# Kernel optimization log

Measured on AMD Instinct MI355X. Metric: run time of the kernel, lower is better.

## Reference

```python
import jax, jax.numpy as jnp
import numpy as np

B, S, HID = 2, 1024, 4096
H, KV, D = 32, 8, 128
EPS = 1e-6
ROPE_THETA = 1000000.0


def _make_freqs_cis(seq_len, head_dim, theta):
    inv_freq = 1.0 / (theta ** (jnp.arange(0, head_dim, 2, dtype=jnp.float32) / head_dim))
    ang = jnp.arange(seq_len, dtype=jnp.float32)[:, None] * inv_freq[None, :]  # [S, D/2]
    emb = jnp.concatenate([ang, ang], axis=-1)                                 # [S, D]
    cos, sin = jnp.cos(emb), jnp.sin(emb)
    return jnp.stack([cos, sin, -sin], axis=0)                                 # [3, S, D]


def setup_inputs() -> dict:
    key = jax.random.key(0)
    ks = jax.random.split(key, 8)
    scale = 0.02
    return {
        "hidden_states": jax.random.normal(ks[0], (B, S, HID), dtype=jnp.float32),
        "freqs_cis": _make_freqs_cis(S, D, ROPE_THETA),
        "Wq": jax.random.normal(ks[1], (H * D, HID), dtype=jnp.float32) * scale,
        "Wk": jax.random.normal(ks[2], (KV * D, HID), dtype=jnp.float32) * scale,
        "Wv": jax.random.normal(ks[3], (KV * D, HID), dtype=jnp.float32) * scale,
        "Wo": jax.random.normal(ks[4], (HID, H * D), dtype=jnp.float32) * scale,
        "q_norm_w": jnp.ones((D,), jnp.float32) + jax.random.normal(ks[5], (D,), jnp.float32) * scale,
        "k_norm_w": jnp.ones((D,), jnp.float32) + jax.random.normal(ks[6], (D,), jnp.float32) * scale,
    }


def _rmsnorm(x, w):
    # per-head RMSNorm over last dim (rms_norm_add=False -> plain weight multiply)
    return x * jax.lax.rsqrt(jnp.mean(x * x, axis=-1, keepdims=True) + EPS) * w


def _rope(x, cos, sin, nsin):
    # matches apply_rope: e = x*cos; e[:half] += x[half:]*nsin; e[half:] += x[:half]*sin
    half = x.shape[-1] // 2
    e = x * cos
    lo = e[..., :half] + x[..., half:] * nsin[..., :half]
    hi = e[..., half:] + x[..., :half] * sin[..., half:]
    return jnp.concatenate([lo, hi], axis=-1)


def reference(hidden_states, freqs_cis, Wq, Wk, Wv, Wo, q_norm_w, k_norm_w):
    b, s, _ = hidden_states.shape
    # QKV projections (no bias)
    q = jnp.einsum("bsh,oh->bso", hidden_states, Wq).reshape(b, s, H, D).transpose(0, 2, 1, 3)
    k = jnp.einsum("bsh,oh->bso", hidden_states, Wk).reshape(b, s, KV, D).transpose(0, 2, 1, 3)
    v = jnp.einsum("bsh,oh->bso", hidden_states, Wv).reshape(b, s, KV, D).transpose(0, 2, 1, 3)
    # per-head RMSNorm (Qwen3 'gemma3' q/k norms)
    q = _rmsnorm(q, q_norm_w)
    k = _rmsnorm(k, k_norm_w)
    # RoPE
    cos, sin, nsin = freqs_cis[0], freqs_cis[1], freqs_cis[2]  # [S, D] each, broadcast over (b, heads)
    q = _rope(q, cos, sin, nsin)
    k = _rope(k, cos, sin, nsin)
    # GQA: repeat kv heads to match query heads (repeat_interleave dim=1)
    rep = H // KV
    k = jnp.repeat(k, rep, axis=1)
    v = jnp.repeat(v, rep, axis=1)
    # SDPA (no mask, past_key_value=None path)
    scale = D ** -0.5
    attn = jax.nn.softmax(jnp.einsum("bhqd,bhkd->bhqk", q, k) * scale, axis=-1)
    out = jnp.einsum("bhqk,bhkd->bhqd", attn, v)
    out = out.transpose(0, 2, 1, 3).reshape(b, s, H * D)
    return jnp.einsum("bsi,hi->bsh", out, Wo)
```

## Files before the change

### kernel.cpp

```cpp
#include <hip/hip_runtime.h>


typedef __attribute__((ext_vector_type(8))) short s8v;
typedef __attribute__((ext_vector_type(4))) float f4v;
typedef __attribute__((ext_vector_type(8))) unsigned short u8v;
typedef __attribute__((ext_vector_type(4))) float float4v;
typedef unsigned short us;

#define SB() __builtin_amdgcn_sched_barrier(0)

__device__ __forceinline__ void BARRIER() {
  asm volatile("" ::: "memory");
  __builtin_amdgcn_s_barrier();
  asm volatile("" ::: "memory");
}

__device__ __forceinline__ us f2b(float f) {
  unsigned u = __builtin_bit_cast(unsigned, f);
  u += 0x7fffu + ((u >> 16) & 1u);
  return (us)(u >> 16);
}
__device__ __forceinline__ float b2f(us h) {
  return __builtin_bit_cast(float, (unsigned)h << 16);
}

__device__ __forceinline__ void gload16(const void* g, void* l) {
  __builtin_amdgcn_global_load_lds(
      (const __attribute__((address_space(1))) unsigned int*)g,
      (__attribute__((address_space(3))) unsigned int*)l, 16, 0, 0);
}

__global__ __launch_bounds__(256) void cvt_all_k(const float* __restrict__ h,
                                                 const float* __restrict__ wq,
                                                 const float* __restrict__ wk,
                                                 const float* __restrict__ wv,
                                                 us* __restrict__ dst) {
  long blk = blockIdx.x;
  const float* src;
  long off;
  if (blk < 4096)        { src = h;  off = 0; }
  else if (blk < 12288)  { src = wq; off = 4096; }
  else if (blk < 14336)  { src = wk; off = 12288; }
  else                   { src = wv; off = 14336; }
  long i = (blk - off) * 2048 + (long)threadIdx.x * 8;
  long o = blk * 2048 + (long)threadIdx.x * 8;
  float4v a = *(const float4v*)(src + i);
  float4v b = *(const float4v*)(src + i + 4);
  u8v v;
  v[0] = f2b(a[0]); v[1] = f2b(a[1]); v[2] = f2b(a[2]); v[3] = f2b(a[3]);
  v[4] = f2b(b[0]); v[5] = f2b(b[1]); v[6] = f2b(b[2]); v[7] = f2b(b[3]);
  *(u8v*)(dst + o) = v;
}

__global__ __launch_bounds__(256) void add2_k(const float* __restrict__ p,
                                              float* __restrict__ out, long n) {
  long i = ((long)blockIdx.x * 256 + threadIdx.x) * 8;
  float4v a0 = *(const float4v*)(p + i);
  float4v b0 = *(const float4v*)(p + i + 4);
  float4v a1 = *(const float4v*)(p + n + i);
  float4v b1 = *(const float4v*)(p + n + i + 4);
  float4v ra, rb;
#pragma unroll
  for (int k = 0; k < 4; ++k) { ra[k] = a0[k] + a1[k]; rb[k] = b0[k] + b1[k]; }
  *(float4v*)(out + i) = ra;
  *(float4v*)(out + i + 4) = rb;
}

template <bool F32OUT, bool SPLITK, bool CVTTAIL>
__global__ __launch_bounds__(512, 2) void gemm8p(const us* __restrict__ A,
                                                 const us* __restrict__ W,
                                                 void* __restrict__ Cv,
                                                 int Kfull, int nkt, int ldc,
                                                 int NX, int nGemm,
                                                 const float* __restrict__ csrc,
                                                 us* __restrict__ cdst) {
  if constexpr (CVTTAIL) {
    if ((int)blockIdx.x >= nGemm) {
      long c = (long)((int)blockIdx.x - nGemm) * 512 + threadIdx.x;
      for (; c < 2097152; c += 64 * 512) {
        long i = c * 8;
        float4v x = *(const float4v*)(csrc + i);
        float4v y = *(const float4v*)(csrc + i + 4);
        u8v v;
        v[0] = f2b(x[0]); v[1] = f2b(x[1]); v[2] = f2b(x[2]); v[3] = f2b(x[3]);
        v[4] = f2b(y[0]); v[5] = f2b(y[1]); v[6] = f2b(y[2]); v[7] = f2b(y[3]);
        *(u8v*)(cdst + i) = v;
      }
      return;
    }
  }

  __shared__ __align__(16) us Ah[2][2][128 * 64];
  __shared__ __align__(16) us Bh[2][2][128 * 64];
  const int tid = threadIdx.x, lane = tid & 63, w = tid >> 6;
  const int wr = w >> 2, wc = w & 3;
  const int lr = lane & 15, lg = lane >> 4;

  const int cpx = nGemm >> 3;
  const int swz = ((int)blockIdx.x & 7) * cpx + ((int)blockIdx.x >> 3);
  long m0, n0, koff = 0;
  float* Cks = (float*)Cv;
  if constexpr (SPLITK) {
    const int ks = swz >> 7;
    const int r = swz & 127;
    m0 = (long)(r >> 4) * 256;
    n0 = (long)(r & 15) * 256;
    koff = (long)ks * nkt * 64;
    Cks += (long)ks * 2048 * 4096;
  } else {
    m0 = (long)(swz / NX) * 256;
    n0 = (long)(swz % NX) * 256;
  }

  const int c0 = tid, c1 = 512 + tid;
  const int r0 = c0 >> 3, r1 = c1 >> 3;
  const int s0 = ((c0 & 7) ^ (r0 & 7)) << 3;
  const int s1 = ((c1 & 7) ^ (r1 & 7)) << 3;

#define STG(dst, src)                                                   \
  do {                                                                  \
    const us* _s = (src);                                               \
    us* _d = (dst);                                                     \
    gload16(_s + (long)r0 * Kfull + s0, _d + c0 * 8);                   \
    gload16(_s + (long)r1 * Kfull + s1, _d + c1 * 8);                   \
  } while (0)

  const us* Asrc = A + m0 * Kfull + koff;
  const us* Bsrc = W + n0 * Kfull + koff;
  const long hK = (long)128 * Kfull;

  const int ra = wr * 64 + lr, rb = wc * 32 + lr;
  const int offA0 = ra * 64 + ((lg ^ (ra & 7)) << 3);
  const int offA1 = ra * 64 + (((4 + lg) ^ (ra & 7)) << 3);
  const int offB0 = rb * 64 + ((lg ^ (rb & 7)) << 3);
  const int offB1 = rb * 64 + (((4 + lg) ^ (rb & 7)) << 3);

  f4v acc[8][4];
#pragma unroll
  for (int i = 0; i < 8; ++i)
#pragma unroll
    for (int j = 0; j < 4; ++j) acc[i][j] = (f4v){0.f, 0.f, 0.f, 0.f};

  const int nk = nkt;

  STG(Ah[0][0], Asrc);
  STG(Bh[0][0], Bsrc);
  STG(Bh[0][1], Bsrc + hK);
  STG(Ah[0][1], Asrc + hK);
  STG(Ah[1][0], Asrc + 64);
  STG(Bh[1][1], Bsrc + hK + 64);
  STG(Ah[1][1], Asrc + hK + 64);
  asm volatile("s_waitcnt vmcnt(6)" ::: "memory");
  BARRIER();

  s8v a[4][2], b0[2][2], b1[2][2];

#define RD_A(H)                                                         \
  _Pragma("unroll") for (int f = 0; f < 4; ++f) {                       \
    a[f][0] = *(const s8v*)(&Ah[d][H][offA0 + f * 1024]);               \
    a[f][1] = *(const s8v*)(&Ah[d][H][offA1 + f * 1024]);               \
  }
#define RD_B(BB, H)                                                     \
  _Pragma("unroll") for (int g = 0; g < 2; ++g) {                       \
    BB[g][0] = *(const s8v*)(&Bh[d][H][offB0 + g * 1024]);              \
    BB[g][1] = *(const s8v*)(&Bh[d][H][offB1 + g * 1024]);              \
  }
#define QUAD(QM, QN, BB)                                                \
  __builtin_amdgcn_s_setprio(1);                                        \
  _Pragma("unroll") for (int f = 0; f < 4; ++f)                         \
  _Pragma("unroll") for (int g = 0; g < 2; ++g) {                       \
    f4v t = acc[QM * 4 + f][QN * 2 + g];                                \
    t = __builtin_amdgcn_mfma_f32_16x16x32_bf16(a[f][0], BB[g][0], t, 0, 0, 0); \
    t = __builtin_amdgcn_mfma_f32_16x16x32_bf16(a[f][1], BB[g][1], t, 0, 0, 0); \
    acc[QM * 4 + f][QN * 2 + g] = t;                                    \
  }                                                                     \
  __builtin_amdgcn_s_setprio(0);
#define PREMFMA()                                                       \
  BARRIER();                                                            \
  asm volatile("s_waitcnt lgkmcnt(0)" ::: "memory");                    \
  SB();

  for (int kt = 0; kt < nk; ++kt) {
    const int d = kt & 1;
    const long kb2 = (long)(kt + 2) * 64;
    const bool p1 = (kt + 1 < nk), p2 = (kt + 2 < nk);

    RD_A(0)
    RD_B(b0, 0)
    if (p1) STG(Bh[d ^ 1][0], Bsrc + (long)(kt + 1) * 64);
    PREMFMA()
    QUAD(0, 0, b0)
    SB(); BARRIER();

    RD_B(b1, 1)
    if (p2) STG(Ah[d][0], Asrc + kb2);
    PREMFMA()
    QUAD(0, 1, b1)
    SB(); BARRIER();

    RD_A(1)
    if (p2) STG(Bh[d][1], Bsrc + hK + kb2);
    PREMFMA()
    QUAD(1, 1, b1)
    SB(); BARRIER();

    if (p2) STG(Ah[d][1], Asrc + hK + kb2);
    PREMFMA()
    QUAD(1, 0, b0)
    SB();
    if (p2) asm volatile("s_waitcnt vmcnt(6)" ::: "memory");
    else    asm volatile("s_waitcnt vmcnt(0)" ::: "memory");
    BARRIER();
  }

#pragma unroll
  for (int qm = 0; qm < 2; ++qm)
#pragma unroll
    for (int f = 0; f < 4; ++f) {
      long row = m0 + qm * 128 + wr * 64 + f * 16 + lg * 4;
#pragma unroll
      for (int qn = 0; qn < 2; ++qn)
#pragma unroll
        for (int g = 0; g < 2; ++g) {
          long col = n0 + qn * 128 + wc * 32 + g * 16 + lr;
          f4v v = acc[qm * 4 + f][qn * 2 + g];
          if constexpr (F32OUT) {
#pragma unroll
            for (int r = 0; r < 4; ++r) Cks[(row + r) * ldc + col] = v[r];
          } else {
            us* C = (us*)Cv;
#pragma unroll
            for (int r = 0; r < 4; ++r) C[(row + r) * ldc + col] = f2b(v[r]);
          }
        }
    }
#undef STG
#undef RD_A
#undef RD_B
#undef QUAD
#undef PREMFMA
}

__global__ __launch_bounds__(256) void rms_rope_k(us* __restrict__ qkv,
                                                  const float* __restrict__ fc,
                                                  const float* __restrict__ qw,
                                                  const float* __restrict__ kw) {
  int idx = blockIdx.x * 4 + (threadIdx.x >> 6);
  int lane = threadIdx.x & 63;
  int head = idx % 40;
  int row = idx / 40;
  int s = row & 1023;
  us* p;
  const float* w;
  if (head < 32) { p = qkv + (long)row * 6144 + head * 128; w = qw; }
  else           { p = qkv + (long)row * 6144 + 4096 + (head - 32) * 128; w = kw; }
  float x0 = b2f(p[lane]), x1 = b2f(p[lane + 64]);
  float ss = x0 * x0 + x1 * x1;
#pragma unroll
  for (int off = 32; off; off >>= 1) ss += __shfl_xor(ss, off);
  float r = rsqrtf(ss * (1.0f / 128.0f) + 1e-6f);
  float y0 = x0 * r * w[lane], y1 = x1 * r * w[lane + 64];
  const float* cosp = fc + (long)s * 128;
  const float* sinp = cosp + 1024 * 128;
  const float* nsinp = sinp + 1024 * 128;
  float e0 = y0 * cosp[lane] + y1 * nsinp[lane];
  float e1 = y1 * cosp[lane + 64] + y0 * sinp[lane + 64];
  p[lane] = f2b(e0);
  p[lane + 64] = f2b(e1);
}

__global__ __launch_bounds__(256) void attn_k(const us* __restrict__ qkv,
                                              us* __restrict__ ao) {
  __shared__ us Kt[64 * 128];
  __shared__ us Vt[128 * 72];
  __shared__ us Pl[4 * 1024];

  const int bid = blockIdx.x;
  const int qt = bid & 15;
  const int h = (bid >> 4) & 31;
  const int b = bid >> 9;
  const int kvh = h >> 2;
  const int tid = threadIdx.x, lane = tid & 63, w = tid >> 6;
  const int lr = lane & 15, lg = lane >> 4;

  const us* Qb =
      qkv + (long)(b * 1024 + qt * 64 + w * 16 + lr) * 6144 + h * 128;
  s8v qf[4];
#pragma unroll
  for (int ks = 0; ks < 4; ++ks) qf[ks] = *(const s8v*)(Qb + ks * 32 + lg * 8);

  f4v o[8];
#pragma unroll
  for (int n = 0; n < 8; ++n) o[n] = (f4v){0.f, 0.f, 0.f, 0.f};
  float m[4], l[4];
#pragma unroll
  for (int r = 0; r < 4; ++r) { m[r] = -1e30f; l[r] = 0.f; }

  const float SL = 0.08838834764831845f * 1.4426950408889634f;
  const long krow = (long)b * 1024 * 6144 + 4096 + kvh * 128;
  const long vrow = (long)b * 1024 * 6144 + 5120 + kvh * 128;

  for (int kt = 0; kt < 16; ++kt) {
    __syncthreads();
#pragma unroll
    for (int t = 0; t < 4; ++t) {
      int c = t * 256 + tid;
      int row = c >> 4;
      int sc = (c & 15) ^ (row & 7);
      gload16(qkv + krow + (long)(kt * 64 + row) * 6144 + sc * 8, &Kt[c * 8]);
    }
#pragma unroll
    for (int t = 0; t < 4; ++t) {
      int c = t * 256 + tid;
      int key = c & 63;
      int d0 = (c >> 6) * 8;
      s8v v = *(const s8v*)(qkv + vrow + (long)(kt * 64 + key) * 6144 + d0);
#pragma unroll
      for (int i = 0; i < 8; ++i) Vt[(d0 + i) * 72 + key] = (us)v[i];
    }
    __syncthreads();

    f4v sacc[4];
#pragma unroll
    for (int j = 0; j < 4; ++j) sacc[j] = (f4v){0.f, 0.f, 0.f, 0.f};
    __builtin_amdgcn_s_setprio(1);
#pragma unroll
    for (int ks = 0; ks < 4; ++ks) {
#pragma unroll
      for (int j = 0; j < 4; ++j) {
        int key = j * 16 + lr;
        s8v kf = *(const s8v*)&Kt[key * 128 + (((ks * 64 + lg * 16) ^ ((key & 7) << 4)) >> 1)];
        sacc[j] = __builtin_amdgcn_mfma_f32_16x16x32_bf16(qf[ks], kf, sacc[j], 0, 0, 0);
      }
    }
    __builtin_amdgcn_s_setprio(0);

    float sm[4];
#pragma unroll
    for (int r = 0; r < 4; ++r)
      sm[r] = fmaxf(fmaxf(sacc[0][r], sacc[1][r]), fmaxf(sacc[2][r], sacc[3][r]));
#pragma unroll
    for (int off = 1; off < 16; off <<= 1)
#pragma unroll
      for (int r = 0; r < 4; ++r) sm[r] = fmaxf(sm[r], __shfl_xor(sm[r], off));
    float alpha[4];
#pragma unroll
    for (int r = 0; r < 4; ++r) {
      float nm = fmaxf(m[r], sm[r] * SL);
      alpha[r] = exp2f(m[r] - nm);
      m[r] = nm;
      l[r] *= alpha[r];
    }
#pragma unroll
    for (int n = 0; n < 8; ++n)
#pragma unroll
      for (int r = 0; r < 4; ++r) o[n][r] *= alpha[r];

    us* pw = Pl + w * 1024;
#pragma unroll
    for (int j = 0; j < 4; ++j)
#pragma unroll
      for (int r = 0; r < 4; ++r) {
        float p = exp2f(sacc[j][r] * SL - m[r]);
        l[r] += p;
        int prow = lg * 4 + r, pcol = j * 16 + lr;
        pw[(prow * 128 + ((pcol * 2) ^ ((prow & 7) << 4))) >> 1] = f2b(p);
      }

    __builtin_amdgcn_s_setprio(1);
#pragma unroll
    for (int ks = 0; ks < 2; ++ks) {
      int bo = ks * 64 + lg * 16;
      s8v pf = *(const s8v*)&Pl[w * 1024 + ((lr * 128 + (bo ^ ((lr & 7) << 4))) >> 1)];
#pragma unroll
      for (int n = 0; n < 8; ++n) {
        s8v vf = *(const s8v*)&Vt[(n * 16 + lr) * 72 + ks * 32 + lg * 8];
        o[n] = __builtin_amdgcn_mfma_f32_16x16x32_bf16(pf, vf, o[n], 0, 0, 0);
      }
    }
    __builtin_amdgcn_s_setprio(0);
  }

#pragma unroll
  for (int off = 1; off < 16; off <<= 1)
#pragma unroll
    for (int r = 0; r < 4; ++r) l[r] += __shfl_xor(l[r], off);
  float inv[4];
#pragma unroll
  for (int r = 0; r < 4; ++r) inv[r] = 1.f / l[r];
  const long ob = (long)(b * 1024 + qt * 64 + w * 16) * 4096 + h * 128;
#pragma unroll
  for (int n = 0; n < 8; ++n)
#pragma unroll
    for (int r = 0; r < 4; ++r)
      ao[ob + (long)(lg * 4 + r) * 4096 + n * 16 + lr] = f2b(o[n][r] * inv[r]);
}

extern "C" void kernel_launch(void* const* d_in, const int* in_sizes, int n_in,
                              void* d_out, int out_size, void* d_ws, size_t ws_size,
                              hipStream_t stream) {
  const float* hidden = (const float*)d_in[0];
  const float* fc     = (const float*)d_in[1];
  const float* Wq     = (const float*)d_in[2];
  const float* Wk     = (const float*)d_in[3];
  const float* Wv     = (const float*)d_in[4];
  const float* Wo     = (const float*)d_in[5];
  const float* qw     = (const float*)d_in[6];
  const float* kw     = (const float*)d_in[7];

  us* hb  = (us*)d_ws;
  us* wb  = hb + (long)2048 * 4096;
  us* wbo = wb + (long)6144 * 4096;
  us* qkv = wbo + (long)4096 * 4096;
  us* ao  = qkv + (long)2048 * 6144;
  float* part = (float*)d_ws;

  cvt_all_k<<<16384, 256, 0, stream>>>(hidden, Wq, Wk, Wv, hb);

  gemm8p<false, false, true><<<256, 512, 0, stream>>>(
      hb, wb, qkv, 4096, 64, 6144, 24, 192, Wo, wbo);

  rms_rope_k<<<20480, 256, 0, stream>>>(qkv, fc, qw, kw);

  attn_k<<<1024, 256, 0, stream>>>(qkv, ao);

  gemm8p<true, true, false><<<256, 512, 0, stream>>>(
      ao, wbo, part, 4096, 32, 4096, 16, 256, nullptr, nullptr);

  add2_k<<<4096, 256, 0, stream>>>(part, (float*)d_out, (long)2048 * 4096);
}
```

Before: 354.4 us.

## Replace split-K output GEMM with half-height tiles and XCD-aware tile mapping

The output projection GEMM drops split-K, which wrote two fp32 partial buffers that a separate add kernel then summed. It now uses 128x256 tiles over the full K and writes fp32 results straight to the output. The GEMM kernel is templated on A-tile height and gets a new block-to-tile mapping that groups tiles per XCD. The RMSNorm+RoPE kernel is vectorized to load and store element pairs, using a lane shuffle to fetch the rotate-half partner. This removes a kernel launch and large partial-sum traffic, at the cost of lower operand reuse per block in the output GEMM.

```diff
diff --git a/kernel.cpp b/kernel.cpp
--- a/kernel.cpp
+++ b/kernel.cpp
@@ -5,6 +5,7 @@
 typedef __attribute__((ext_vector_type(4))) float f4v;
 typedef __attribute__((ext_vector_type(8))) unsigned short u8v;
 typedef __attribute__((ext_vector_type(4))) float float4v;
+typedef __attribute__((ext_vector_type(2))) float float2v;
 typedef unsigned short us;
 
 #define SB() __builtin_amdgcn_sched_barrier(0)
@@ -52,26 +53,13 @@
   *(u8v*)(dst + o) = v;
 }
 
-__global__ __launch_bounds__(256) void add2_k(const float* __restrict__ p,
-                                              float* __restrict__ out, long n) {
-  long i = ((long)blockIdx.x * 256 + threadIdx.x) * 8;
-  float4v a0 = *(const float4v*)(p + i);
-  float4v b0 = *(const float4v*)(p + i + 4);
-  float4v a1 = *(const float4v*)(p + n + i);
-  float4v b1 = *(const float4v*)(p + n + i + 4);
-  float4v ra, rb;
-#pragma unroll
-  for (int k = 0; k < 4; ++k) { ra[k] = a0[k] + a1[k]; rb[k] = b0[k] + b1[k]; }
-  *(float4v*)(out + i) = ra;
-  *(float4v*)(out + i + 4) = rb;
-}
-
-template <bool F32OUT, bool SPLITK, bool CVTTAIL>
+template <int AH, bool F32OUT, bool CVTTAIL>
 __global__ __launch_bounds__(512, 2) void gemm8p(const us* __restrict__ A,
                                                  const us* __restrict__ W,
                                                  void* __restrict__ Cv,
-                                                 int Kfull, int nkt, int ldc,
-                                                 int NX, int nGemm,
+                                                 int K, int nkt, int ldc,
+                                                 int cm, int cn, int ncn,
+                                                 int nGemm,
                                                  const float* __restrict__ csrc,
                                                  us* __restrict__ cdst) {
   if constexpr (CVTTAIL) {
@@ -90,73 +78,66 @@
     }
   }
 
-  __shared__ __align__(16) us Ah[2][2][128 * 64];
+  constexpr int FR = AH / 32;
+  constexpr int LA = AH / 64;
+  constexpr int VM = 2 * LA + 2;
+
+  __shared__ __align__(16) us Ah[2][2][AH * 64];
   __shared__ __align__(16) us Bh[2][2][128 * 64];
   const int tid = threadIdx.x, lane = tid & 63, w = tid >> 6;
   const int wr = w >> 2, wc = w & 3;
   const int lr = lane & 15, lg = lane >> 4;
 
-  const int cpx = nGemm >> 3;
-  const int swz = ((int)blockIdx.x & 7) * cpx + ((int)blockIdx.x >> 3);
-  long m0, n0, koff = 0;
-  float* Cks = (float*)Cv;
-  if constexpr (SPLITK) {
-    const int ks = swz >> 7;
-    const int r = swz & 127;
-    m0 = (long)(r >> 4) * 256;
-    n0 = (long)(r & 15) * 256;
-    koff = (long)ks * nkt * 64;
-    Cks += (long)ks * 2048 * 4096;
-  } else {
-    m0 = (long)(swz / NX) * 256;
-    n0 = (long)(swz % NX) * 256;
-  }
-
-  const int c0 = tid, c1 = 512 + tid;
-  const int r0 = c0 >> 3, r1 = c1 >> 3;
-  const int s0 = ((c0 & 7) ^ (r0 & 7)) << 3;
-  const int s1 = ((c1 & 7) ^ (r1 & 7)) << 3;
-
-#define STG(dst, src)                                                   \
+  const int xcd = (int)blockIdx.x & 7;
+  const int i2 = (int)blockIdx.x >> 3;
+  const int im = i2 % cm, itn = i2 / cm;
+  const long m0 = (long)((xcd / ncn) * cm + im) * (2 * AH);
+  const long n0 = (long)((xcd % ncn) * cn + itn) * 256;
+
+  const int rA0 = tid >> 3;
+  const int sc0 = ((tid & 7) ^ (rA0 & 7)) << 3;
+
+#define STGH(dst, src, LOADS)                                           \
   do {                                                                  \
     const us* _s = (src);                                               \
     us* _d = (dst);                                                     \
-    gload16(_s + (long)r0 * Kfull + s0, _d + c0 * 8);                   \
-    gload16(_s + (long)r1 * Kfull + s1, _d + c1 * 8);                   \
+    _Pragma("unroll") for (int l = 0; l < (LOADS); ++l)                 \
+      gload16(_s + (long)(rA0 + l * 64) * K + sc0, _d + (l * 512 + tid) * 8); \
   } while (0)
 
-  const us* Asrc = A + m0 * Kfull + koff;
-  const us* Bsrc = W + n0 * Kfull + koff;
-  const long hK = (long)128 * Kfull;
-
-  const int ra = wr * 64 + lr, rb = wc * 32 + lr;
+  const us* Asrc = A + m0 * K;
+  const us* Bsrc = W + n0 * K;
+  const long hKA = (long)AH * K;
+  const long hKB = (long)128 * K;
+
+  const int ra = wr * (AH / 2) + lr, rb = wc * 32 + lr;
   const int offA0 = ra * 64 + ((lg ^ (ra & 7)) << 3);
   const int offA1 = ra * 64 + (((4 + lg) ^ (ra & 7)) << 3);
   const int offB0 = rb * 64 + ((lg ^ (rb & 7)) << 3);
   const int offB1 = rb * 64 + (((4 + lg) ^ (rb & 7)) << 3);
 
-  f4v acc[8][4];
-#pragma unroll
-  for (int i = 0; i < 8; ++i)
+  f4v acc[2 * FR][4];
+#pragma unroll
+  for (int i = 0; i < 2 * FR; ++i)
 #pragma unroll
     for (int j = 0; j < 4; ++j) acc[i][j] = (f4v){0.f, 0.f, 0.f, 0.f};
 
   const int nk = nkt;
 
-  STG(Ah[0][0], Asrc);
-  STG(Bh[0][0], Bsrc);
-  STG(Bh[0][1], Bsrc + hK);
-  STG(Ah[0][1], Asrc + hK);
-  STG(Ah[1][0], Asrc + 64);
-  STG(Bh[1][1], Bsrc + hK + 64);
-  STG(Ah[1][1], Asrc + hK + 64);
-  asm volatile("s_waitcnt vmcnt(6)" ::: "memory");
+  STGH(Ah[0][0], Asrc, LA);
+  STGH(Bh[0][0], Bsrc, 2);
+  STGH(Bh[0][1], Bsrc + hKB, 2);
+  STGH(Ah[0][1], Asrc + hKA, LA);
+  STGH(Ah[1][0], Asrc + 64, LA);
+  STGH(Bh[1][1], Bsrc + hKB + 64, 2);
+  STGH(Ah[1][1], Asrc + hKA + 64, LA);
+  asm volatile("s_waitcnt vmcnt(%0)" :: "i"(VM) : "memory");
   BARRIER();
 
-  s8v a[4][2], b0[2][2], b1[2][2];
+  s8v a[FR][2], b0[2][2], b1[2][2];
 
 #define RD_A(H)                                                         \
-  _Pragma("unroll") for (int f = 0; f < 4; ++f) {                       \
+  _Pragma("unroll") for (int f = 0; f < FR; ++f) {                      \
     a[f][0] = *(const s8v*)(&Ah[d][H][offA0 + f * 1024]);               \
     a[f][1] = *(const s8v*)(&Ah[d][H][offA1 + f * 1024]);               \
   }
@@ -167,12 +148,12 @@
   }
 #define QUAD(QM, QN, BB)                                                \
   __builtin_amdgcn_s_setprio(1);                                        \
-  _Pragma("unroll") for (int f = 0; f < 4; ++f)                         \
+  _Pragma("unroll") for (int f = 0; f < FR; ++f)                        \
   _Pragma("unroll") for (int g = 0; g < 2; ++g) {                       \
-    f4v t = acc[QM * 4 + f][QN * 2 + g];                                \
+    f4v t = acc[QM * FR + f][QN * 2 + g];                               \
     t = __builtin_amdgcn_mfma_f32_16x16x32_bf16(a[f][0], BB[g][0], t, 0, 0, 0); \
     t = __builtin_amdgcn_mfma_f32_16x16x32_bf16(a[f][1], BB[g][1], t, 0, 0, 0); \
-    acc[QM * 4 + f][QN * 2 + g] = t;                                    \
+    acc[QM * FR + f][QN * 2 + g] = t;                                   \
   }                                                                     \
   __builtin_amdgcn_s_setprio(0);
 #define PREMFMA()                                                       \
@@ -187,28 +168,28 @@
 
     RD_A(0)
     RD_B(b0, 0)
-    if (p1) STG(Bh[d ^ 1][0], Bsrc + (long)(kt + 1) * 64);
+    if (p1) STGH(Bh[d ^ 1][0], Bsrc + (long)(kt + 1) * 64, 2);
     PREMFMA()
     QUAD(0, 0, b0)
     SB(); BARRIER();
 
     RD_B(b1, 1)
-    if (p2) STG(Ah[d][0], Asrc + kb2);
+    if (p2) STGH(Ah[d][0], Asrc + kb2, LA);
     PREMFMA()
     QUAD(0, 1, b1)
     SB(); BARRIER();
 
     RD_A(1)
-    if (p2) STG(Bh[d][1], Bsrc + hK + kb2);
+    if (p2) STGH(Bh[d][1], Bsrc + hKB + kb2, 2);
     PREMFMA()
     QUAD(1, 1, b1)
     SB(); BARRIER();
 
-    if (p2) STG(Ah[d][1], Asrc + hK + kb2);
+    if (p2) STGH(Ah[d][1], Asrc + hKA + kb2, LA);
     PREMFMA()
     QUAD(1, 0, b0)
     SB();
-    if (p2) asm volatile("s_waitcnt vmcnt(6)" ::: "memory");
+    if (p2) asm volatile("s_waitcnt vmcnt(%0)" :: "i"(VM) : "memory");
     else    asm volatile("s_waitcnt vmcnt(0)" ::: "memory");
     BARRIER();
   }
@@ -216,17 +197,18 @@
 #pragma unroll
   for (int qm = 0; qm < 2; ++qm)
 #pragma unroll
-    for (int f = 0; f < 4; ++f) {
-      long row = m0 + qm * 128 + wr * 64 + f * 16 + lg * 4;
+    for (int f = 0; f < FR; ++f) {
+      long row = m0 + qm * AH + wr * (AH / 2) + f * 16 + lg * 4;
 #pragma unroll
       for (int qn = 0; qn < 2; ++qn)
 #pragma unroll
         for (int g = 0; g < 2; ++g) {
           long col = n0 + qn * 128 + wc * 32 + g * 16 + lr;
-          f4v v = acc[qm * 4 + f][qn * 2 + g];
+          f4v v = acc[qm * FR + f][qn * 2 + g];
           if constexpr (F32OUT) {
-#pragma unroll
-            for (int r = 0; r < 4; ++r) Cks[(row + r) * ldc + col] = v[r];
+            float* C = (float*)Cv;
+#pragma unroll
+            for (int r = 0; r < 4; ++r) C[(row + r) * ldc + col] = v[r];
           } else {
             us* C = (us*)Cv;
 #pragma unroll
@@ -234,7 +216,7 @@
           }
         }
     }
-#undef STG
+#undef STGH
 #undef RD_A
 #undef RD_B
 #undef QUAD
@@ -254,19 +236,23 @@
   const float* w;
   if (head < 32) { p = qkv + (long)row * 6144 + head * 128; w = qw; }
   else           { p = qkv + (long)row * 6144 + 4096 + (head - 32) * 128; w = kw; }
-  float x0 = b2f(p[lane]), x1 = b2f(p[lane + 64]);
+
+  unsigned v = ((const unsigned*)p)[lane];
+  float x0 = b2f((us)(v & 0xffff)), x1 = b2f((us)(v >> 16));
   float ss = x0 * x0 + x1 * x1;
 #pragma unroll
   for (int off = 32; off; off >>= 1) ss += __shfl_xor(ss, off);
   float r = rsqrtf(ss * (1.0f / 128.0f) + 1e-6f);
-  float y0 = x0 * r * w[lane], y1 = x1 * r * w[lane + 64];
-  const float* cosp = fc + (long)s * 128;
-  const float* sinp = cosp + 1024 * 128;
-  const float* nsinp = sinp + 1024 * 128;
-  float e0 = y0 * cosp[lane] + y1 * nsinp[lane];
-  float e1 = y1 * cosp[lane + 64] + y0 * sinp[lane + 64];
-  p[lane] = f2b(e0);
-  p[lane + 64] = f2b(e1);
+  float2v wv = ((const float2v*)w)[lane];
+  float y0 = x0 * r * wv[0], y1 = x1 * r * wv[1];
+  float py0 = __shfl(y0, lane ^ 32);
+  float py1 = __shfl(y1, lane ^ 32);
+  float2v cv = ((const float2v*)(fc + (long)s * 128))[lane];
+  const float* sbase = (lane < 32) ? (fc + 2 * 1024 * 128) : (fc + 1024 * 128);
+  float2v sv = ((const float2v*)(sbase + (long)s * 128))[lane];
+  float e0 = y0 * cv[0] + py0 * sv[0];
+  float e1 = y1 * cv[1] + py1 * sv[1];
+  ((unsigned*)p)[lane] = (unsigned)f2b(e0) | ((unsigned)f2b(e1) << 16);
 }
 
 __global__ __launch_bounds__(256) void attn_k(const us* __restrict__ qkv,
@@ -413,19 +399,16 @@
   us* wbo = wb + (long)6144 * 4096;
   us* qkv = wbo + (long)4096 * 4096;
   us* ao  = qkv + (long)2048 * 6144;
-  float* part = (float*)d_ws;
 
   cvt_all_k<<<16384, 256, 0, stream>>>(hidden, Wq, Wk, Wv, hb);
 
-  gemm8p<false, false, true><<<256, 512, 0, stream>>>(
-      hb, wb, qkv, 4096, 64, 6144, 24, 192, Wo, wbo);
+  gemm8p<128, false, true><<<256, 512, 0, stream>>>(
+      hb, wb, qkv, 4096, 64, 6144, 4, 6, 4, 192, Wo, wbo);
 
   rms_rope_k<<<20480, 256, 0, stream>>>(qkv, fc, qw, kw);
 
   attn_k<<<1024, 256, 0, stream>>>(qkv, ao);
 
-  gemm8p<true, true, false><<<256, 512, 0, stream>>>(
-      ao, wbo, part, 4096, 32, 4096, 16, 256, nullptr, nullptr);
-
-  add2_k<<<4096, 256, 0, stream>>>(part, (float*)d_out, (long)2048 * 4096);
-}
+  gemm8p<64, true, false><<<256, 512, 0, stream>>>(
+      ao, wbo, d_out, 4096, 64, 4096, 8, 4, 4, 256, nullptr, nullptr);
+}
```

Result: faster. 345.2 us (-2.6%).
